# Kernel tuning notes

Hardware: AMD Instinct MI355X
Metric: run time of the kernel (lower is better)

The kernel has to match this reference:

```python
import jax, jax.numpy as jnp
import numpy as np

NUM_HEADS = 16


def setup_inputs() -> dict:
    key = jax.random.key(0)
    ks = jax.random.split(key, 5)
    B, N, D = 2, 2048, 1024
    scale = 1.0 / np.sqrt(D)  # roughly xavier-ish magnitude for weights
    return {
        "x": jax.random.normal(ks[0], (B, N, D), dtype=jnp.float32),
        "W_query": jax.random.normal(ks[1], (D, D), dtype=jnp.float32) * scale,
        "W_key": jax.random.normal(ks[2], (D, D), dtype=jnp.float32) * scale,
        "W_value": jax.random.normal(ks[3], (D, D), dtype=jnp.float32) * scale,
        "W_output": jax.random.normal(ks[4], (D, D), dtype=jnp.float32) * scale,
    }


def reference(x, W_query, W_key, W_value, W_output):
    # x: [B, N, D]; weights: [D, D]
    B, N, D = x.shape
    H = NUM_HEADS
    hd = D // H

    def mh_embed(W):
        # linear_embedding then split heads: [B, N, D] -> [B, H, N, hd]
        y = jnp.einsum("bnd,de->bne", x, W)
        return y.reshape(B, N, H, hd).transpose(0, 2, 1, 3)

    q = mh_embed(W_query)
    k = mh_embed(W_key)
    v = mh_embed(W_value)

    # NOTE: source scales by token_dim**-0.5 (full model dim), not head_dim
    attn = jnp.einsum("bhnd,bhmd->bhnm", q, k) * (D ** -0.5)
    attn = jax.nn.softmax(attn, axis=-1)
    out = jnp.einsum("bhnm,bhmd->bhnd", attn, v)  # [B, H, N, hd]

    out = out.transpose(0, 2, 1, 3).reshape(B, N, D)  # merge heads
    out = jnp.einsum("bnd,de->bne", out, W_output)
    return out
```

## Files before the change

kernel.cpp:

```cpp
#include <hip/hip_runtime.h>

#define D_MODEL 1024
#define N_TOK   2048
#define NHEAD   16
#define HDIM    64
#define BATCH   2
#define M_TOT   (BATCH*N_TOK)

typedef unsigned short u16;
typedef __bf16 bf16x8 __attribute__((ext_vector_type(8)));
typedef float  f32x4  __attribute__((ext_vector_type(4)));

#define QSCALE 0.04508422002777439f

__device__ __forceinline__ u16 f2bf(float f) {
  union { float f; unsigned u; } v; v.f = f;
  unsigned r = v.u + 0x7fffu + ((v.u >> 16) & 1u);
  return (u16)(r >> 16);
}

__device__ __forceinline__ float bf2f(u16 u) {
  union { unsigned u; float f; } v; v.u = ((unsigned)u) << 16; return v.f;
}

__device__ __forceinline__ unsigned pk2bf(float a, float b) {
#if __has_builtin(__builtin_amdgcn_cvt_pk_bf16_f32)
  typedef __bf16 bf16x2_t __attribute__((ext_vector_type(2)));
  bf16x2_t r = __builtin_amdgcn_cvt_pk_bf16_f32(a, b);
  union { bf16x2_t v; unsigned u; } c; c.v = r; return c.u;
#else
  return (unsigned)f2bf(a) | ((unsigned)f2bf(b) << 16);
#endif
}

__device__ __forceinline__ unsigned comb2(unsigned a, unsigned b, float inv) {
  float x = (bf2f((u16)(a & 0xffff)) + bf2f((u16)(b & 0xffff))) * inv;
  float y = (bf2f((u16)(a >> 16))   + bf2f((u16)(b >> 16)))   * inv;
  return pk2bf(x, y);
}

__device__ __forceinline__ void gl2lds16(const void* g, void* l) {
  __builtin_amdgcn_global_load_lds(
      (__attribute__((address_space(1))) void*)g,
      (__attribute__((address_space(3))) void*)l, 16, 0, 0);
}

__global__ void prep_kernel(const float* __restrict__ x,
                            const float* __restrict__ s0, const float* __restrict__ s1,
                            const float* __restrict__ s2, const float* __restrict__ s3,
                            u16* __restrict__ xb,
                            u16* __restrict__ d0, u16* __restrict__ d1,
                            u16* __restrict__ d2, u16* __restrict__ d3) {
  const int t = threadIdx.y * 32 + threadIdx.x;
  if (blockIdx.z == 4) {
    int base = (blockIdx.y * 32 + blockIdx.x) * 256 + t;
#pragma unroll
    for (int r = 0; r < 4; ++r) {
      int i = base + r * 262144;
      float4 v = ((const float4*)x)[i];
      ushort4 o;
      o.x = f2bf(v.x); o.y = f2bf(v.y); o.z = f2bf(v.z); o.w = f2bf(v.w);
      ((ushort4*)xb)[i] = o;
    }
    return;
  }
  const float* src; u16* dst;
  switch (blockIdx.z) {
    case 0:  src = s0; dst = d0; break;
    case 1:  src = s1; dst = d1; break;
    case 2:  src = s2; dst = d2; break;
    default: src = s3; dst = d3; break;
  }
  float sc = (blockIdx.z == 0) ? QSCALE : 1.0f;
  __shared__ float tile[32][33];
  int xg = blockIdx.x * 32 + threadIdx.x;
  int ybase = blockIdx.y * 32;
#pragma unroll
  for (int r = 0; r < 4; ++r)
    tile[threadIdx.y + r*8][threadIdx.x] = src[(size_t)(ybase + threadIdx.y + r*8)*D_MODEL + xg];
  __syncthreads();
#pragma unroll
  for (int r = 0; r < 4; ++r)
    dst[(size_t)(blockIdx.x*32 + threadIdx.y + r*8)*D_MODEL + ybase + threadIdx.x] =
        f2bf(tile[threadIdx.x][threadIdx.y + r*8] * sc);
}

__device__ __forceinline__ void gemm_body(const u16* __restrict__ A,
                                          const u16* __restrict__ Bt,
                                          void* __restrict__ Cout, int mode) {
  __shared__ __attribute__((aligned(16))) u16 lA[2][128*32];
  __shared__ __attribute__((aligned(16))) u16 lB[2][128*32];
  const int t = threadIdx.x;
  const int lane = t & 63, w = t >> 6;
  const int wm = w >> 1, wn = w & 1;
  const int q4 = lane >> 4, l15 = lane & 15;
  const int m0 = blockIdx.y * 128, n0 = blockIdx.x * 128;

  const int c0 = t, c1 = 256 + t;
  const int r0 = c0 >> 2, g0 = (c0 & 3) ^ (r0 & 3);
  const int r1 = c1 >> 2, g1 = (c1 & 3) ^ (r1 & 3);

  f32x4 acc[4][4] = {};

  gl2lds16(A  + (size_t)(m0 + r0)*D_MODEL + g0*8, &lA[0][c0*8]);
  gl2lds16(Bt + (size_t)(n0 + r0)*D_MODEL + g0*8, &lB[0][c0*8]);
  gl2lds16(A  + (size_t)(m0 + r1)*D_MODEL + g1*8, &lA[0][c1*8]);
  gl2lds16(Bt + (size_t)(n0 + r1)*D_MODEL + g1*8, &lB[0][c1*8]);

  for (int it = 0; it < 32; ++it) {
    const int cur = it & 1;
    __syncthreads();
    if (it + 1 < 32) {
      const int kn = (it + 1) * 32;
      u16* dA = &lA[cur ^ 1][0]; u16* dB = &lB[cur ^ 1][0];
      gl2lds16(A  + (size_t)(m0 + r0)*D_MODEL + kn + g0*8, dA + c0*8);
      gl2lds16(Bt + (size_t)(n0 + r0)*D_MODEL + kn + g0*8, dB + c0*8);
      gl2lds16(A  + (size_t)(m0 + r1)*D_MODEL + kn + g1*8, dA + c1*8);
      gl2lds16(Bt + (size_t)(n0 + r1)*D_MODEL + kn + g1*8, dB + c1*8);
    }
    const u16* sA = &lA[cur][0]; const u16* sB = &lB[cur][0];
    bf16x8 af[4], bfr[4];
#pragma unroll
    for (int mi = 0; mi < 4; ++mi) {
      int r = wm*64 + mi*16 + l15;
      af[mi] = *(const bf16x8*)(sA + r*32 + ((q4 ^ (r & 3)) * 8));
    }
#pragma unroll
    for (int ni = 0; ni < 4; ++ni) {
      int r = wn*64 + ni*16 + l15;
      bfr[ni] = *(const bf16x8*)(sB + r*32 + ((q4 ^ (r & 3)) * 8));
    }
#pragma unroll
    for (int mi = 0; mi < 4; ++mi)
#pragma unroll
      for (int ni = 0; ni < 4; ++ni)
        acc[mi][ni] = __builtin_amdgcn_mfma_f32_16x16x32_bf16(af[mi], bfr[ni], acc[mi][ni], 0, 0, 0);
  }

#pragma unroll
  for (int mi = 0; mi < 4; ++mi) {
#pragma unroll
    for (int ni = 0; ni < 4; ++ni) {
      const int tok0 = m0 + wm*64 + mi*16 + q4*4;
      const int col  = n0 + wn*64 + ni*16 + l15;
      if (mode == 0) {
        u16* D = (u16*)Cout;
#pragma unroll
        for (int r = 0; r < 4; ++r) {
          int tok = tok0 + r;
          int b = tok >> 11, n = tok & (N_TOK-1);
          int h = col >> 6, d = col & (HDIM-1);
          D[(((size_t)(b*NHEAD + h))*N_TOK + n)*HDIM + d] = f2bf(acc[mi][ni][r]);
        }
      } else {
        int b = tok0 >> 11, n = tok0 & (N_TOK-1);
        int h = col >> 6, d = col & (HDIM-1);
        ushort4 pk;
        pk.x = f2bf(acc[mi][ni][0]); pk.y = f2bf(acc[mi][ni][1]);
        pk.z = f2bf(acc[mi][ni][2]); pk.w = f2bf(acc[mi][ni][3]);
        *(ushort4*)((u16*)Cout + ((size_t)(b*NHEAD + h)*HDIM + d)*N_TOK + n) = pk;
      }
    }
  }
}

__global__ __launch_bounds__(256) void qkv_kernel(const u16* __restrict__ xb,
    const u16* __restrict__ wqt, const u16* __restrict__ wkt, const u16* __restrict__ wvt,
    u16* __restrict__ Q, u16* __restrict__ K, u16* __restrict__ Vt) {
  int z = blockIdx.z;
  const u16* B = (z == 0) ? wqt : (z == 1) ? wkt : wvt;
  void* C = (z == 0) ? (void*)Q : (z == 1) ? (void*)K : (void*)Vt;
  gemm_body(xb, B, C, (z == 2) ? 2 : 0);
}

__global__ __launch_bounds__(256) void out_kernel(const u16* __restrict__ Op,
    const float* __restrict__ Lp, const u16* __restrict__ wot,
    float* __restrict__ out) {
  __shared__ __attribute__((aligned(16))) u16 lA[2][64*32];
  __shared__ __attribute__((aligned(16))) u16 lB[2][128*32];
  const int t = threadIdx.x;
  const int lane = t & 63, w = t >> 6;
  const int wm = w >> 1, wn = w & 1;
  const int q4 = lane >> 4, l15 = lane & 15;
  const int m0 = blockIdx.y * 64, n0 = blockIdx.x * 128;

  const int rA = t >> 2, gA = (t & 3) ^ (rA & 3);
  const int tok = m0 + rA;
  const int nA = tok & (N_TOK-1), bA = tok >> 11;
  const int c0 = t, c1 = 256 + t;
  const int r0 = c0 >> 2, g0 = (c0 & 3) ^ (r0 & 3);
  const int r1 = c1 >> 2, g1 = (c1 & 3) ^ (r1 & 3);

  f32x4 acc[2][4] = {};
  uint4 pa, pb;
  float l0, l1;

  {
    const size_t off = (size_t)tok*D_MODEL + gA*8;
    pa = *(const uint4*)(Op + off);
    pb = *(const uint4*)(Op + (size_t)(M_TOT*D_MODEL) + off);
    l0 = Lp[(size_t)(bA*NHEAD)*N_TOK + nA];
    l1 = Lp[(size_t)(32*N_TOK) + (size_t)(bA*NHEAD)*N_TOK + nA];
    gl2lds16(wot + (size_t)(n0 + r0)*D_MODEL + g0*8, &lB[0][c0*8]);
    gl2lds16(wot + (size_t)(n0 + r1)*D_MODEL + g1*8, &lB[0][c1*8]);
    float inv = 1.0f / (l0 + l1);
    uint4 o;
    o.x = comb2(pa.x, pb.x, inv); o.y = comb2(pa.y, pb.y, inv);
    o.z = comb2(pa.z, pb.z, inv); o.w = comb2(pa.w, pb.w, inv);
    *(uint4*)(&lA[0][t*8]) = o;
  }

  for (int it = 0; it < 32; ++it) {
    const int cur = it & 1;
    __syncthreads();
    const bool hasNext = (it + 1) < 32;
    if (hasNext) {
      const int kn = (it + 1) * 32;
      const int h2 = (it + 1) >> 1;
      const size_t off = (size_t)tok*D_MODEL + kn + gA*8;
      pa = *(const uint4*)(Op + off);
      pb = *(const uint4*)(Op + (size_t)(M_TOT*D_MODEL) + off);
      l0 = Lp[(size_t)(bA*NHEAD + h2)*N_TOK + nA];
      l1 = Lp[(size_t)(32*N_TOK) + (size_t)(bA*NHEAD + h2)*N_TOK + nA];
      u16* dB = &lB[cur ^ 1][0];
      gl2lds16(wot + (size_t)(n0 + r0)*D_MODEL + kn + g0*8, dB + c0*8);
      gl2lds16(wot + (size_t)(n0 + r1)*D_MODEL + kn + g1*8, dB + c1*8);
    }
    const u16* sA = &lA[cur][0]; const u16* sB = &lB[cur][0];
    bf16x8 af[2], bfr[4];
#pragma unroll
    for (int mi = 0; mi < 2; ++mi) {
      int r = wm*32 + mi*16 + l15;
      af[mi] = *(const bf16x8*)(sA + r*32 + ((q4 ^ (r & 3)) * 8));
    }
#pragma unroll
    for (int ni = 0; ni < 4; ++ni) {
      int r = wn*64 + ni*16 + l15;
      bfr[ni] = *(const bf16x8*)(sB + r*32 + ((q4 ^ (r & 3)) * 8));
    }
#pragma unroll
    for (int mi = 0; mi < 2; ++mi)
#pragma unroll
      for (int ni = 0; ni < 4; ++ni)
        acc[mi][ni] = __builtin_amdgcn_mfma_f32_16x16x32_bf16(af[mi], bfr[ni], acc[mi][ni], 0, 0, 0);
    if (hasNext) {
      float inv = 1.0f / (l0 + l1);
      uint4 o;
      o.x = comb2(pa.x, pb.x, inv); o.y = comb2(pa.y, pb.y, inv);
      o.z = comb2(pa.z, pb.z, inv); o.w = comb2(pa.w, pb.w, inv);
      *(uint4*)(&lA[cur ^ 1][t*8]) = o;
    }
  }

#pragma unroll
  for (int mi = 0; mi < 2; ++mi) {
#pragma unroll
    for (int ni = 0; ni < 4; ++ni) {
      const int tok0 = m0 + wm*32 + mi*16 + q4*4;
      const int col  = n0 + wn*64 + ni*16 + l15;
#pragma unroll
      for (int r = 0; r < 4; ++r)
        out[(size_t)(tok0 + r)*D_MODEL + col] = acc[mi][ni][r];
    }
  }
}

__global__ __launch_bounds__(256, 4) void attn_kernel(const u16* __restrict__ Qg,
    const u16* __restrict__ Kg, const u16* __restrict__ Vtg,
    u16* __restrict__ Opart, float* __restrict__ Lpart) {
  __shared__ __attribute__((aligned(16))) u16 lds[16384];
  const int t = threadIdx.x;
  const int lane = t & 63, w = t >> 6;
  const int q4 = lane >> 4, l15 = lane & 15;
  const int bh = blockIdx.y;
  const int qb = blockIdx.x >> 1, sp = blockIdx.x & 1;
  const int qw0 = qb * 128 + w * 32;
  const size_t kvBase = (size_t)bh * (N_TOK * HDIM);
  u16* myP = lds + 8192 + w * 2048;

  const int ck0 = t, ck1 = 256 + t;
  const int kr0 = ck0 >> 3, kg0 = (ck0 & 7) ^ (kr0 & 7);
  const int kr1 = ck1 >> 3, kg1 = (ck1 & 7) ^ (kr1 & 7);

  bf16x8 qf[2][2];
#pragma unroll
  for (int ni = 0; ni < 2; ++ni)
#pragma unroll
    for (int kk = 0; kk < 2; ++kk)
      qf[ni][kk] = *(const bf16x8*)(Qg + kvBase +
                    (size_t)(qw0 + ni*16 + l15)*HDIM + kk*32 + q4*8);

  f32x4 accO[4][2] = {};
  float lsum[2] = {0.f, 0.f};

  const int kvStart = sp * 1024;
  for (int it = 0; it < 16; ++it) {
    const int kv0 = kvStart + it * 64;
    __syncthreads();
    gl2lds16(Kg  + kvBase + (size_t)(kv0 + kr0)*HDIM + kg0*8, lds + ck0*8);
    gl2lds16(Kg  + kvBase + (size_t)(kv0 + kr1)*HDIM + kg1*8, lds + ck1*8);
    gl2lds16(Vtg + kvBase + (size_t)kr0*N_TOK + kv0 + kg0*8,  lds + 4096 + ck0*8);
    gl2lds16(Vtg + kvBase + (size_t)kr1*N_TOK + kv0 + kg1*8,  lds + 4096 + ck1*8);
    __syncthreads();

#pragma unroll
    for (int mip = 0; mip < 4; ++mip) {
      const int kv = mip*16 + l15;
      f32x4 s[2] = {};
#pragma unroll
      for (int kk = 0; kk < 2; ++kk) {
        bf16x8 a = *(const bf16x8*)(lds + kv*64 + (((kk*4 + q4) ^ (l15 & 7)) * 8));
#pragma unroll
        for (int ni = 0; ni < 2; ++ni)
          s[ni] = __builtin_amdgcn_mfma_f32_16x16x32_bf16(a, qf[ni][kk], s[ni], 0, 0, 0);
      }
#pragma unroll
      for (int ni = 0; ni < 2; ++ni) {
        float p0 = __builtin_amdgcn_exp2f(s[ni][0]);
        float p1 = __builtin_amdgcn_exp2f(s[ni][1]);
        float p2 = __builtin_amdgcn_exp2f(s[ni][2]);
        float p3 = __builtin_amdgcn_exp2f(s[ni][3]);
        lsum[ni] += (p0 + p1) + (p2 + p3);
        uint2 u; u.x = pk2bf(p0, p1); u.y = pk2bf(p2, p3);
        const int qloc = ni*16 + l15;
        const int kv8 = mip*4 + q4;
        *(uint2*)(myP + qloc*64 + (((kv8 >> 1) ^ (qloc & 7)) * 8) + (kv8 & 1)*4) = u;
      }
    }

#pragma unroll
    for (int kk2 = 0; kk2 < 2; ++kk2) {
      bf16x8 bp[2];
#pragma unroll
      for (int ni = 0; ni < 2; ++ni)
        bp[ni] = *(const bf16x8*)(myP + (ni*16 + l15)*64 +
                                  (((kk2*4 + q4) ^ (l15 & 7)) * 8));
#pragma unroll
      for (int mi2 = 0; mi2 < 4; ++mi2) {
        const int d = mi2*16 + l15;
        bf16x8 av = *(const bf16x8*)(lds + 4096 + d*64 +
                                     (((kk2*4 + q4) ^ (d & 7)) * 8));
#pragma unroll
        for (int ni = 0; ni < 2; ++ni)
          accO[mi2][ni] = __builtin_amdgcn_mfma_f32_16x16x32_bf16(av, bp[ni], accO[mi2][ni], 0, 0, 0);
      }
    }
  }

  const int b = bh >> 4, head = bh & (NHEAD-1);
  u16* Obase = Opart + (size_t)sp * (M_TOT * D_MODEL);
#pragma unroll
  for (int ni = 0; ni < 2; ++ni) {
    float ls = lsum[ni];
    ls += __shfl_xor(ls, 16);
    ls += __shfl_xor(ls, 32);
    const int q = qw0 + ni*16 + l15;
    if (q4 == 0)
      Lpart[(size_t)sp*(32*N_TOK) + bh*N_TOK + q] = ls;
    const size_t rb = ((size_t)(b*N_TOK + q))*D_MODEL + head*HDIM + q4*4;
#pragma unroll
    for (int mi2 = 0; mi2 < 4; ++mi2) {
      uint2 u;
      u.x = pk2bf(accO[mi2][ni][0], accO[mi2][ni][1]);
      u.y = pk2bf(accO[mi2][ni][2], accO[mi2][ni][3]);
      *(uint2*)(Obase + rb + mi2*16) = u;
    }
  }
}

extern "C" void kernel_launch(void* const* d_in, const int* in_sizes, int n_in,
                              void* d_out, int out_size, void* d_ws, size_t ws_size,
                              hipStream_t stream) {
  const float* x  = (const float*)d_in[0];
  const float* Wq = (const float*)d_in[1];
  const float* Wk = (const float*)d_in[2];
  const float* Wv = (const float*)d_in[3];
  const float* Wo = (const float*)d_in[4];
  float* out = (float*)d_out;

  char* ws = (char*)d_ws;
  u16* xb   = (u16*)(ws);
  u16* wqt  = (u16*)(ws + (8u  << 20));
  u16* wkt  = (u16*)(ws + (10u << 20));
  u16* wvt  = (u16*)(ws + (12u << 20));
  u16* wot  = (u16*)(ws + (14u << 20));
  u16* Qw   = (u16*)(ws + (16u << 20));
  u16* Kw   = (u16*)(ws + (24u << 20));
  u16* Vtw  = (u16*)(ws + (32u << 20));
  u16* Op   = (u16*)(ws + (40u << 20));
  float* Lp = (float*)(ws);
  (void)in_sizes; (void)n_in; (void)out_size; (void)ws_size;

  prep_kernel<<<dim3(32, 32, 5), dim3(32, 8), 0, stream>>>(x, Wq, Wk, Wv, Wo,
                                                           xb, wqt, wkt, wvt, wot);
  qkv_kernel<<<dim3(8, 32, 3), 256, 0, stream>>>(xb, wqt, wkt, wvt, Qw, Kw, Vtw);
  attn_kernel<<<dim3(32, 32), 256, 0, stream>>>(Qw, Kw, Vtw, Op, Lp);
  out_kernel<<<dim3(8, 64), 256, 0, stream>>>(Op, Lp, wot, out);
}
```

Measured before the change: 207.1 us.

## Stage QKV GEMM epilogue through LDS for coalesced stores, transpose V separately

The QKV GEMM epilogue now writes bf16 results into a swizzled shared-memory tile and then stores full 16-byte head rows, replacing scattered 2-byte stores. V is written in the same [B,H,N,hd] layout as Q and K, and a new small kernel transposes it into the Vt layout the attention kernel expects. This aims to cut uncoalesced global write traffic in the GEMM, at the cost of an extra kernel launch and an extra read and write of V.

```diff
diff --git a/kernel.cpp b/kernel.cpp
--- a/kernel.cpp
+++ b/kernel.cpp
@@ -87,9 +87,8 @@
 
 __device__ __forceinline__ void gemm_body(const u16* __restrict__ A,
                                           const u16* __restrict__ Bt,
-                                          void* __restrict__ Cout, int mode) {
-  __shared__ __attribute__((aligned(16))) u16 lA[2][128*32];
-  __shared__ __attribute__((aligned(16))) u16 lB[2][128*32];
+                                          u16* __restrict__ D) {
+  __shared__ __attribute__((aligned(16))) u16 sm[16384];
   const int t = threadIdx.x;
   const int lane = t & 63, w = t >> 6;
   const int wm = w >> 1, wn = w & 1;
@@ -102,23 +101,25 @@
 
   f32x4 acc[4][4] = {};
 
-  gl2lds16(A  + (size_t)(m0 + r0)*D_MODEL + g0*8, &lA[0][c0*8]);
-  gl2lds16(Bt + (size_t)(n0 + r0)*D_MODEL + g0*8, &lB[0][c0*8]);
-  gl2lds16(A  + (size_t)(m0 + r1)*D_MODEL + g1*8, &lA[0][c1*8]);
-  gl2lds16(Bt + (size_t)(n0 + r1)*D_MODEL + g1*8, &lB[0][c1*8]);
+  gl2lds16(A  + (size_t)(m0 + r0)*D_MODEL + g0*8, sm + c0*8);
+  gl2lds16(Bt + (size_t)(n0 + r0)*D_MODEL + g0*8, sm + 8192 + c0*8);
+  gl2lds16(A  + (size_t)(m0 + r1)*D_MODEL + g1*8, sm + c1*8);
+  gl2lds16(Bt + (size_t)(n0 + r1)*D_MODEL + g1*8, sm + 8192 + c1*8);
 
   for (int it = 0; it < 32; ++it) {
     const int cur = it & 1;
     __syncthreads();
     if (it + 1 < 32) {
       const int kn = (it + 1) * 32;
-      u16* dA = &lA[cur ^ 1][0]; u16* dB = &lB[cur ^ 1][0];
+      u16* dA = sm + (cur ^ 1) * 4096;
+      u16* dB = sm + 8192 + (cur ^ 1) * 4096;
       gl2lds16(A  + (size_t)(m0 + r0)*D_MODEL + kn + g0*8, dA + c0*8);
       gl2lds16(Bt + (size_t)(n0 + r0)*D_MODEL + kn + g0*8, dB + c0*8);
       gl2lds16(A  + (size_t)(m0 + r1)*D_MODEL + kn + g1*8, dA + c1*8);
       gl2lds16(Bt + (size_t)(n0 + r1)*D_MODEL + kn + g1*8, dB + c1*8);
     }
-    const u16* sA = &lA[cur][0]; const u16* sB = &lB[cur][0];
+    const u16* sA = sm + cur * 4096;
+    const u16* sB = sm + 8192 + cur * 4096;
     bf16x8 af[4], bfr[4];
 #pragma unroll
     for (int mi = 0; mi < 4; ++mi) {
@@ -137,40 +138,59 @@
         acc[mi][ni] = __builtin_amdgcn_mfma_f32_16x16x32_bf16(af[mi], bfr[ni], acc[mi][ni], 0, 0, 0);
   }
 
-#pragma unroll
-  for (int mi = 0; mi < 4; ++mi) {
+  __syncthreads();
+#pragma unroll
+  for (int mi = 0; mi < 4; ++mi)
 #pragma unroll
     for (int ni = 0; ni < 4; ++ni) {
-      const int tok0 = m0 + wm*64 + mi*16 + q4*4;
-      const int col  = n0 + wn*64 + ni*16 + l15;
-      if (mode == 0) {
-        u16* D = (u16*)Cout;
-#pragma unroll
-        for (int r = 0; r < 4; ++r) {
-          int tok = tok0 + r;
-          int b = tok >> 11, n = tok & (N_TOK-1);
-          int h = col >> 6, d = col & (HDIM-1);
-          D[(((size_t)(b*NHEAD + h))*N_TOK + n)*HDIM + d] = f2bf(acc[mi][ni][r]);
-        }
-      } else {
-        int b = tok0 >> 11, n = tok0 & (N_TOK-1);
-        int h = col >> 6, d = col & (HDIM-1);
-        ushort4 pk;
-        pk.x = f2bf(acc[mi][ni][0]); pk.y = f2bf(acc[mi][ni][1]);
-        pk.z = f2bf(acc[mi][ni][2]); pk.w = f2bf(acc[mi][ni][3]);
-        *(ushort4*)((u16*)Cout + ((size_t)(b*NHEAD + h)*HDIM + d)*N_TOK + n) = pk;
+      const int row0 = wm*64 + mi*16 + q4*4;
+      const int col  = wn*64 + ni*16 + l15;
+      const int ch = col >> 3, c7 = col & 7;
+#pragma unroll
+      for (int r = 0; r < 4; ++r) {
+        const int row = row0 + r;
+        sm[row*128 + ((ch ^ (row & 15)) * 8) + c7] = f2bf(acc[mi][ni][r]);
       }
+    }
+  __syncthreads();
+  {
+    const int tokL = t & 127, h = t >> 7;
+    const int tokG = m0 + tokL;
+    const int b = tokG >> 11, n = tokG & (N_TOK-1);
+    const int hg = (n0 >> 6) + h;
+    u16* dst = D + (((size_t)(b*NHEAD + hg))*N_TOK + n)*HDIM;
+#pragma unroll
+    for (int ch = 0; ch < 8; ++ch) {
+      uint4 v = *(const uint4*)(sm + tokL*128 + (((h*8 + ch) ^ (tokL & 15)) * 8));
+      *(uint4*)(dst + ch*8) = v;
     }
   }
 }
 
 __global__ __launch_bounds__(256) void qkv_kernel(const u16* __restrict__ xb,
     const u16* __restrict__ wqt, const u16* __restrict__ wkt, const u16* __restrict__ wvt,
-    u16* __restrict__ Q, u16* __restrict__ K, u16* __restrict__ Vt) {
+    u16* __restrict__ Q, u16* __restrict__ K, u16* __restrict__ V) {
   int z = blockIdx.z;
   const u16* B = (z == 0) ? wqt : (z == 1) ? wkt : wvt;
-  void* C = (z == 0) ? (void*)Q : (z == 1) ? (void*)K : (void*)Vt;
-  gemm_body(xb, B, C, (z == 2) ? 2 : 0);
+  u16* C = (z == 0) ? Q : (z == 1) ? K : V;
+  gemm_body(xb, B, C);
+}
+
+__global__ void vtrans_kernel(const u16* __restrict__ V, u16* __restrict__ Vt) {
+  __shared__ u16 tile[32][34];
+  const int bh = blockIdx.z;
+  const int n0 = blockIdx.x * 32, d0 = blockIdx.y * 32;
+  const u16* src = V + ((size_t)bh*N_TOK + n0)*HDIM + d0;
+  u16* dst = Vt + ((size_t)bh*HDIM + d0)*N_TOK + n0;
+#pragma unroll
+  for (int r = 0; r < 4; ++r)
+    tile[threadIdx.y + r*8][threadIdx.x] =
+        src[(size_t)(threadIdx.y + r*8)*HDIM + threadIdx.x];
+  __syncthreads();
+#pragma unroll
+  for (int r = 0; r < 4; ++r)
+    dst[(size_t)(threadIdx.y + r*8)*N_TOK + threadIdx.x] =
+        tile[threadIdx.x][threadIdx.y + r*8];
 }
 
 __global__ __launch_bounds__(256) void out_kernel(const u16* __restrict__ Op,
@@ -386,14 +406,16 @@
   u16* wot  = (u16*)(ws + (14u << 20));
   u16* Qw   = (u16*)(ws + (16u << 20));
   u16* Kw   = (u16*)(ws + (24u << 20));
-  u16* Vtw  = (u16*)(ws + (32u << 20));
-  u16* Op   = (u16*)(ws + (40u << 20));
+  u16* Vw   = (u16*)(ws + (32u << 20));
+  u16* Vtw  = (u16*)(ws + (40u << 20));
+  u16* Op   = (u16*)(ws + (48u << 20));
   float* Lp = (float*)(ws);
   (void)in_sizes; (void)n_in; (void)out_size; (void)ws_size;
 
   prep_kernel<<<dim3(32, 32, 5), dim3(32, 8), 0, stream>>>(x, Wq, Wk, Wv, Wo,
                                                            xb, wqt, wkt, wvt, wot);
-  qkv_kernel<<<dim3(8, 32, 3), 256, 0, stream>>>(xb, wqt, wkt, wvt, Qw, Kw, Vtw);
+  qkv_kernel<<<dim3(8, 32, 3), 256, 0, stream>>>(xb, wqt, wkt, wvt, Qw, Kw, Vw);
+  vtrans_kernel<<<dim3(64, 2, 32), dim3(32, 8), 0, stream>>>(Vw, Vtw);
   attn_kernel<<<dim3(32, 32), 256, 0, stream>>>(Qw, Kw, Vtw, Op, Lp);
   out_kernel<<<dim3(8, 64), 256, 0, stream>>>(Op, Lp, wot, out);
 }
```

After: 209.1 us. Within noise of the previous version (+1.0%).
